# Kernel optimization log

Measured on AMD Instinct MI355X. Metric: run time of the kernel, lower is better.

The kernel has to match this reference:

```python
import jax, jax.numpy as jnp
import numpy as np

B, T, C, H, W = 4, 5, 64, 48, 48
F = 10                      # num_feat
N = T * H * W               # 11520, ffnn1 is Linear(N, N)


def setup_inputs() -> dict:
    key = jax.random.key(0)
    ks = jax.random.split(key, 9)
    sc = lambda *shape: 1.0 / np.sqrt(shape[-1])
    return {
        "input": jax.random.normal(ks[0], (B, T, C, H, W), jnp.float32),
        "input1": jax.random.normal(ks[1], (1,), jnp.float32),
        "act_weights": jax.random.uniform(ks[2], (3,), jnp.float32),
        # conv1: Conv1d(C, F, 1) -> weight [F, C] (kernel dim squeezed), bias [F]
        "conv1_w": jax.random.normal(ks[3], (F, C), jnp.float32) * sc(F, C),
        "conv1_b": jax.random.normal(ks[4], (F,), jnp.float32) * 0.01,
        # G3: Conv1d(C, F, 1)
        "g3_w": jax.random.normal(ks[5], (F, C), jnp.float32) * sc(F, C),
        "g3_b": jax.random.normal(ks[6], (F,), jnp.float32) * 0.01,
        # ffnn1: Linear(N, N)
        "ffnn_w": jax.random.normal(ks[7], (N, N), jnp.float32) * sc(N, N),
        "ffnn_b": jax.random.normal(ks[8], (N,), jnp.float32) * 0.01,
    }


def reference(input, input1, act_weights, conv1_w, conv1_b, g3_w, g3_b, ffnn_w, ffnn_b):
    b, t, c, h, w = input.shape
    n = t * h * w
    # [B, C, N]: transpose(1,2) then flatten T,H,W
    x = jnp.transpose(input, (0, 2, 1, 3, 4)).reshape(b, c, n)

    # conv1 (1x1) -> [B, F, N]; AvgPool1d(F) over the feat dim -> [B, N]
    c1 = jnp.einsum('bcn,fc->bfn', x, conv1_w) + conv1_b[None, :, None]
    s = jnp.mean(c1, axis=1)                      # [B, N]

    # ffnn1 (same Linear used in all three branches in the original)
    z = s @ ffnn_w.T + ffnn_b                     # [B, N]

    # G3 projection -> [B, N, F]
    g3 = jnp.einsum('bcn,fc->bnf', x, g3_w) + g3_b[None, None, :]

    # diag_embed(z) @ g3^T is exactly a per-position scale of g3 by z.
    gate = (act_weights[0] * jax.nn.relu(z)
            + act_weights[1] * jax.nn.sigmoid(z)
            + act_weights[2] * jax.nn.softmax(z, axis=1))  # [B, N]
    out = gate[:, :, None] * g3                   # [B, N, F]

    out = out.reshape(b, t, h, w, g3.shape[-1])   # [B, T, H, W, F]
    return jnp.transpose(out, (0, 1, 4, 2, 3))    # [B, T, F, H, W]
```

## Files before the change

kernel.cpp:

```cpp
#include <hip/hip_runtime.h>
#include <math.h>

#define Bsz 4
#define Tsz 5
#define Csz 64
#define Fsz 10
#define Hsz 48
#define Wsz 48
#define HWsz (Hsz*Wsz)
#define Nsz (Tsz*HWsz)

#define O_CWM 0
#define O_CBM 64
#define O_S   80
#define O_G3  (O_S + Bsz*Nsz)
#define O_Z   (O_G3 + Bsz*Fsz*Nsz)
#define O_MX  (O_Z + Bsz*Nsz)
#define O_SM  (O_MX + 4)

__global__ void k_prep(const float* __restrict__ cw, const float* __restrict__ cb,
                       float* __restrict__ ws) {
    int c = threadIdx.x;
    if (c < Csz) {
        float acc = 0.f;
        #pragma unroll
        for (int f = 0; f < Fsz; ++f) acc += cw[f*Csz + c];
        ws[O_CWM + c] = acc * (1.0f/Fsz);
    }
    if (c == 0) {
        float acc = 0.f;
        #pragma unroll
        for (int f = 0; f < Fsz; ++f) acc += cb[f];
        ws[O_CBM] = acc * (1.0f/Fsz);
    }
}

__global__ __launch_bounds__(64) void k_sg3(const float* __restrict__ in,
                                            const float* __restrict__ g3w,
                                            const float* __restrict__ g3b,
                                            float* __restrict__ ws) {
    __shared__ float sw[Fsz*Csz];
    __shared__ float scw[Csz + 1];
    for (int i = threadIdx.x; i < Fsz*Csz; i += 64) sw[i] = g3w[i];
    if (threadIdx.x < Csz) scw[threadIdx.x] = ws[O_CWM + threadIdx.x];
    if (threadIdx.x == 0) scw[Csz] = ws[O_CBM];
    __syncthreads();

    const int n = blockIdx.x * 64 + threadIdx.x;
    const int b = blockIdx.y;
    const int t = n / HWsz;
    const int p = n - t * HWsz;

    const float* xp = in + ((size_t)(b*Tsz + t) * Csz) * HWsz + p;

    float accs = 0.f;
    float accf[Fsz];
    #pragma unroll
    for (int f = 0; f < Fsz; ++f) accf[f] = 0.f;

    for (int c = 0; c < Csz; ++c) {
        float xv = xp[(size_t)c * HWsz];
        accs = fmaf(xv, scw[c], accs);
        #pragma unroll
        for (int f = 0; f < Fsz; ++f) accf[f] = fmaf(xv, sw[f*Csz + c], accf[f]);
    }

    float* s   = ws + O_S;
    float* g3t = ws + O_G3;
    s[b*Nsz + n] = accs + scw[Csz];
    #pragma unroll
    for (int f = 0; f < Fsz; ++f)
        g3t[((size_t)b*Fsz + f) * Nsz + n] = accf[f] + g3b[f];
}

__global__ __launch_bounds__(256) void k_gemv(const float* __restrict__ Wm,
                                              const float* __restrict__ fb,
                                              const float* __restrict__ ws) {
    const int wave = threadIdx.x >> 6;
    const int lane = threadIdx.x & 63;
    const int i = blockIdx.x * 4 + wave;

    const float4* wrow = (const float4*)(Wm + (size_t)i * Nsz);
    const float4* s4   = (const float4*)(ws + O_S);
    const int n4c = Nsz / 4;

    float a0 = 0.f, a1 = 0.f, a2 = 0.f, a3 = 0.f;
    for (int j = 0; j < Nsz/256; ++j) {
        const int n4 = j*64 + lane;
        float4 w4 = wrow[n4];
        float4 sv;
        sv = s4[0*n4c + n4];
        a0 = fmaf(w4.x, sv.x, a0); a0 = fmaf(w4.y, sv.y, a0);
        a0 = fmaf(w4.z, sv.z, a0); a0 = fmaf(w4.w, sv.w, a0);
        sv = s4[1*n4c + n4];
        a1 = fmaf(w4.x, sv.x, a1); a1 = fmaf(w4.y, sv.y, a1);
        a1 = fmaf(w4.z, sv.z, a1); a1 = fmaf(w4.w, sv.w, a1);
        sv = s4[2*n4c + n4];
        a2 = fmaf(w4.x, sv.x, a2); a2 = fmaf(w4.y, sv.y, a2);
        a2 = fmaf(w4.z, sv.z, a2); a2 = fmaf(w4.w, sv.w, a2);
        sv = s4[3*n4c + n4];
        a3 = fmaf(w4.x, sv.x, a3); a3 = fmaf(w4.y, sv.y, a3);
        a3 = fmaf(w4.z, sv.z, a3); a3 = fmaf(w4.w, sv.w, a3);
    }
    #pragma unroll
    for (int off = 32; off > 0; off >>= 1) {
        a0 += __shfl_xor(a0, off, 64);
        a1 += __shfl_xor(a1, off, 64);
        a2 += __shfl_xor(a2, off, 64);
        a3 += __shfl_xor(a3, off, 64);
    }
    if (lane == 0) {
        float bias = fb[i];
        float* z = (float*)ws + O_Z;
        z[0*Nsz + i] = a0 + bias;
        z[1*Nsz + i] = a1 + bias;
        z[2*Nsz + i] = a2 + bias;
        z[3*Nsz + i] = a3 + bias;
    }
}

__global__ __launch_bounds__(256) void k_stats(float* __restrict__ ws) {
    const int b = blockIdx.x;
    const float* zb = (const float*)ws + O_Z + (size_t)b * Nsz;
    const int lane = threadIdx.x & 63;
    const int wave = threadIdx.x >> 6;
    __shared__ float red[4];
    __shared__ float bcast;

    float m = -INFINITY;
    for (int i = threadIdx.x; i < Nsz; i += 256) m = fmaxf(m, zb[i]);
    #pragma unroll
    for (int off = 32; off > 0; off >>= 1) m = fmaxf(m, __shfl_xor(m, off, 64));
    if (lane == 0) red[wave] = m;
    __syncthreads();
    if (threadIdx.x == 0)
        bcast = fmaxf(fmaxf(red[0], red[1]), fmaxf(red[2], red[3]));
    __syncthreads();
    m = bcast;

    float sum = 0.f;
    for (int i = threadIdx.x; i < Nsz; i += 256) sum += expf(zb[i] - m);
    #pragma unroll
    for (int off = 32; off > 0; off >>= 1) sum += __shfl_xor(sum, off, 64);
    if (lane == 0) red[wave] = sum;
    __syncthreads();
    if (threadIdx.x == 0) {
        float* mx = ws + O_MX;
        float* sm = ws + O_SM;
        mx[b] = m;
        sm[b] = red[0] + red[1] + red[2] + red[3];
    }
}

__global__ __launch_bounds__(256) void k_out(const float* __restrict__ aw,
                                             const float* __restrict__ ws,
                                             float* __restrict__ out) {
    const int n = blockIdx.x * 256 + threadIdx.x;
    const int b = blockIdx.y;

    const float* z  = ws + O_Z;
    const float zv  = z[(size_t)b*Nsz + n];
    const float a0 = aw[0], a1 = aw[1], a2 = aw[2];
    const float mxb = ws[O_MX + b];
    const float smb = ws[O_SM + b];

    const float gate = a0 * fmaxf(zv, 0.f)
                     + a1 / (1.f + expf(-zv))
                     + a2 * expf(zv - mxb) / smb;

    const int t = n / HWsz;
    const int p = n - t * HWsz;
    const float* gp = ws + O_G3 + (size_t)b * Fsz * Nsz + n;
    float* ob = out + ((size_t)(b*Tsz + t) * Fsz) * HWsz + p;
    #pragma unroll
    for (int f = 0; f < Fsz; ++f)
        ob[(size_t)f * HWsz] = gate * gp[(size_t)f * Nsz];
}

extern "C" void kernel_launch(void* const* d_in, const int* in_sizes, int n_in,
                              void* d_out, int out_size, void* d_ws, size_t ws_size,
                              hipStream_t stream) {
    const float* input  = (const float*)d_in[0];
    const float* aw     = (const float*)d_in[2];
    const float* conv1w = (const float*)d_in[3];
    const float* conv1b = (const float*)d_in[4];
    const float* g3w    = (const float*)d_in[5];
    const float* g3b    = (const float*)d_in[6];
    const float* ffnw   = (const float*)d_in[7];
    const float* ffnb   = (const float*)d_in[8];
    float* out = (float*)d_out;
    float* ws  = (float*)d_ws;

    k_prep<<<1, 64, 0, stream>>>(conv1w, conv1b, ws);
    k_sg3<<<dim3(Nsz/64, Bsz), 64, 0, stream>>>(input, g3w, g3b, ws);
    k_gemv<<<Nsz/4, 256, 0, stream>>>(ffnw, ffnb, ws);
    k_stats<<<Bsz, 256, 0, stream>>>(ws);
    k_out<<<dim3(Nsz/256, Bsz), 256, 0, stream>>>(aw, ws, out);
}
```

Baseline: 769.7 us.

## Tile GEMV over rows with LDS-staged input vector and nontemporal weight loads

Each wave of the GEMV now computes four output rows, and each block stages chunks of the four batch vectors in shared memory. Those vectors are then reused across sixteen rows instead of being reread from global memory for every row. Weight rows are streamed with nontemporal loads. The prep kernel is folded into the projection kernel, which now uses 256-thread blocks, removing one launch. The cost is more registers and block-level syncs per chunk.

New measurement: 686.2 us. -10.9%, faster.

```diff
diff --git a/kernel.cpp b/kernel.cpp
--- a/kernel.cpp
+++ b/kernel.cpp
@@ -9,44 +9,42 @@
 #define Wsz 48
 #define HWsz (Hsz*Wsz)
 #define Nsz (Tsz*HWsz)
-
-#define O_CWM 0
-#define O_CBM 64
-#define O_S   80
+#define N4  (Nsz/4)
+#define KC4 576
+#define NCHUNK 5
+
+typedef float float4n __attribute__((ext_vector_type(4)));
+
+#define O_S   0
 #define O_G3  (O_S + Bsz*Nsz)
 #define O_Z   (O_G3 + Bsz*Fsz*Nsz)
 #define O_MX  (O_Z + Bsz*Nsz)
 #define O_SM  (O_MX + 4)
 
-__global__ void k_prep(const float* __restrict__ cw, const float* __restrict__ cb,
-                       float* __restrict__ ws) {
-    int c = threadIdx.x;
-    if (c < Csz) {
-        float acc = 0.f;
-        #pragma unroll
-        for (int f = 0; f < Fsz; ++f) acc += cw[f*Csz + c];
-        ws[O_CWM + c] = acc * (1.0f/Fsz);
-    }
-    if (c == 0) {
-        float acc = 0.f;
-        #pragma unroll
-        for (int f = 0; f < Fsz; ++f) acc += cb[f];
-        ws[O_CBM] = acc * (1.0f/Fsz);
-    }
-}
-
-__global__ __launch_bounds__(64) void k_sg3(const float* __restrict__ in,
-                                            const float* __restrict__ g3w,
-                                            const float* __restrict__ g3b,
-                                            float* __restrict__ ws) {
+__global__ __launch_bounds__(256) void k_sg3(const float* __restrict__ in,
+                                             const float* __restrict__ cw,
+                                             const float* __restrict__ cb,
+                                             const float* __restrict__ g3w,
+                                             const float* __restrict__ g3b,
+                                             float* __restrict__ ws) {
     __shared__ float sw[Fsz*Csz];
     __shared__ float scw[Csz + 1];
-    for (int i = threadIdx.x; i < Fsz*Csz; i += 64) sw[i] = g3w[i];
-    if (threadIdx.x < Csz) scw[threadIdx.x] = ws[O_CWM + threadIdx.x];
-    if (threadIdx.x == 0) scw[Csz] = ws[O_CBM];
-    __syncthreads();
-
-    const int n = blockIdx.x * 64 + threadIdx.x;
+    if (threadIdx.x < Csz) {
+        float a = 0.f;
+        #pragma unroll
+        for (int f = 0; f < Fsz; ++f) a += cw[f*Csz + threadIdx.x];
+        scw[threadIdx.x] = a * (1.0f/Fsz);
+    }
+    if (threadIdx.x == 0) {
+        float a = 0.f;
+        #pragma unroll
+        for (int f = 0; f < Fsz; ++f) a += cb[f];
+        scw[Csz] = a * (1.0f/Fsz);
+    }
+    for (int i = threadIdx.x; i < Fsz*Csz; i += 256) sw[i] = g3w[i];
+    __syncthreads();
+
+    const int n = blockIdx.x * 256 + threadIdx.x;
     const int b = blockIdx.y;
     const int t = n / HWsz;
     const int p = n - t * HWsz;
@@ -73,49 +71,84 @@
         g3t[((size_t)b*Fsz + f) * Nsz + n] = accf[f] + g3b[f];
 }
 
+#define DOT4(ACC, WV, SV) \
+    ACC = fmaf(WV.x, SV.x, ACC); ACC = fmaf(WV.y, SV.y, ACC); \
+    ACC = fmaf(WV.z, SV.z, ACC); ACC = fmaf(WV.w, SV.w, ACC)
+
 __global__ __launch_bounds__(256) void k_gemv(const float* __restrict__ Wm,
                                               const float* __restrict__ fb,
-                                              const float* __restrict__ ws) {
-    const int wave = threadIdx.x >> 6;
-    const int lane = threadIdx.x & 63;
-    const int i = blockIdx.x * 4 + wave;
-
-    const float4* wrow = (const float4*)(Wm + (size_t)i * Nsz);
-    const float4* s4   = (const float4*)(ws + O_S);
-    const int n4c = Nsz / 4;
-
-    float a0 = 0.f, a1 = 0.f, a2 = 0.f, a3 = 0.f;
-    for (int j = 0; j < Nsz/256; ++j) {
-        const int n4 = j*64 + lane;
-        float4 w4 = wrow[n4];
-        float4 sv;
-        sv = s4[0*n4c + n4];
-        a0 = fmaf(w4.x, sv.x, a0); a0 = fmaf(w4.y, sv.y, a0);
-        a0 = fmaf(w4.z, sv.z, a0); a0 = fmaf(w4.w, sv.w, a0);
-        sv = s4[1*n4c + n4];
-        a1 = fmaf(w4.x, sv.x, a1); a1 = fmaf(w4.y, sv.y, a1);
-        a1 = fmaf(w4.z, sv.z, a1); a1 = fmaf(w4.w, sv.w, a1);
-        sv = s4[2*n4c + n4];
-        a2 = fmaf(w4.x, sv.x, a2); a2 = fmaf(w4.y, sv.y, a2);
-        a2 = fmaf(w4.z, sv.z, a2); a2 = fmaf(w4.w, sv.w, a2);
-        sv = s4[3*n4c + n4];
-        a3 = fmaf(w4.x, sv.x, a3); a3 = fmaf(w4.y, sv.y, a3);
-        a3 = fmaf(w4.z, sv.z, a3); a3 = fmaf(w4.w, sv.w, a3);
-    }
-    #pragma unroll
-    for (int off = 32; off > 0; off >>= 1) {
-        a0 += __shfl_xor(a0, off, 64);
-        a1 += __shfl_xor(a1, off, 64);
-        a2 += __shfl_xor(a2, off, 64);
-        a3 += __shfl_xor(a3, off, 64);
-    }
+                                              float* __restrict__ ws) {
+    __shared__ float4 slds[Bsz][KC4];
+    const int tid  = threadIdx.x;
+    const int wave = tid >> 6;
+    const int lane = tid & 63;
+    const int row0 = blockIdx.x * 16 + wave * 4;
+
+    const float4n* w0 = (const float4n*)(Wm + (size_t)(row0    ) * Nsz);
+    const float4n* w1 = (const float4n*)(Wm + (size_t)(row0 + 1) * Nsz);
+    const float4n* w2 = (const float4n*)(Wm + (size_t)(row0 + 2) * Nsz);
+    const float4n* w3 = (const float4n*)(Wm + (size_t)(row0 + 3) * Nsz);
+    const float4* s4 = (const float4*)(ws + O_S);
+
+    float acc[4][4];
+    #pragma unroll
+    for (int r = 0; r < 4; ++r)
+        #pragma unroll
+        for (int b = 0; b < 4; ++b) acc[r][b] = 0.f;
+
+    for (int ch = 0; ch < NCHUNK; ++ch) {
+        const int c0 = ch * KC4;
+        __syncthreads();
+        #pragma unroll
+        for (int k = 0; k < (Bsz*KC4)/256; ++k) {
+            const int q = k*256 + tid;
+            const int b = q / KC4;
+            const int j = q - b * KC4;
+            slds[b][j] = s4[(size_t)b * N4 + c0 + j];
+        }
+        __syncthreads();
+
+        #pragma unroll
+        for (int jj = 0; jj < KC4/64; ++jj) {
+            const int j  = jj*64 + lane;
+            const int n4 = c0 + j;
+            const float4n a0 = __builtin_nontemporal_load(w0 + n4);
+            const float4n a1 = __builtin_nontemporal_load(w1 + n4);
+            const float4n a2 = __builtin_nontemporal_load(w2 + n4);
+            const float4n a3 = __builtin_nontemporal_load(w3 + n4);
+            float4 sv;
+            sv = slds[0][j];
+            DOT4(acc[0][0], a0, sv); DOT4(acc[1][0], a1, sv);
+            DOT4(acc[2][0], a2, sv); DOT4(acc[3][0], a3, sv);
+            sv = slds[1][j];
+            DOT4(acc[0][1], a0, sv); DOT4(acc[1][1], a1, sv);
+            DOT4(acc[2][1], a2, sv); DOT4(acc[3][1], a3, sv);
+            sv = slds[2][j];
+            DOT4(acc[0][2], a0, sv); DOT4(acc[1][2], a1, sv);
+            DOT4(acc[2][2], a2, sv); DOT4(acc[3][2], a3, sv);
+            sv = slds[3][j];
+            DOT4(acc[0][3], a0, sv); DOT4(acc[1][3], a1, sv);
+            DOT4(acc[2][3], a2, sv); DOT4(acc[3][3], a3, sv);
+        }
+    }
+
+    #pragma unroll
+    for (int r = 0; r < 4; ++r)
+        #pragma unroll
+        for (int b = 0; b < 4; ++b)
+            #pragma unroll
+            for (int off = 32; off > 0; off >>= 1)
+                acc[r][b] += __shfl_xor(acc[r][b], off, 64);
+
     if (lane == 0) {
-        float bias = fb[i];
-        float* z = (float*)ws + O_Z;
-        z[0*Nsz + i] = a0 + bias;
-        z[1*Nsz + i] = a1 + bias;
-        z[2*Nsz + i] = a2 + bias;
-        z[3*Nsz + i] = a3 + bias;
+        float* z = ws + O_Z;
+        #pragma unroll
+        for (int r = 0; r < 4; ++r) {
+            const float bias = fb[row0 + r];
+            #pragma unroll
+            for (int b = 0; b < 4; ++b)
+                z[(size_t)b*Nsz + row0 + r] = acc[r][b] + bias;
+        }
     }
 }
 
@@ -145,10 +178,8 @@
     if (lane == 0) red[wave] = sum;
     __syncthreads();
     if (threadIdx.x == 0) {
-        float* mx = ws + O_MX;
-        float* sm = ws + O_SM;
-        mx[b] = m;
-        sm[b] = red[0] + red[1] + red[2] + red[3];
+        ws[O_MX + b] = m;
+        ws[O_SM + b] = red[0] + red[1] + red[2] + red[3];
     }
 }
 
@@ -158,8 +189,7 @@
     const int n = blockIdx.x * 256 + threadIdx.x;
     const int b = blockIdx.y;
 
-    const float* z  = ws + O_Z;
-    const float zv  = z[(size_t)b*Nsz + n];
+    const float zv  = ws[O_Z + (size_t)b*Nsz + n];
     const float a0 = aw[0], a1 = aw[1], a2 = aw[2];
     const float mxb = ws[O_MX + b];
     const float smb = ws[O_SM + b];
@@ -191,9 +221,8 @@
     float* out = (float*)d_out;
     float* ws  = (float*)d_ws;
 
-    k_prep<<<1, 64, 0, stream>>>(conv1w, conv1b, ws);
-    k_sg3<<<dim3(Nsz/64, Bsz), 64, 0, stream>>>(input, g3w, g3b, ws);
-    k_gemv<<<Nsz/4, 256, 0, stream>>>(ffnw, ffnb, ws);
+    k_sg3  <<<dim3(Nsz/256, Bsz), 256, 0, stream>>>(input, conv1w, conv1b, g3w, g3b, ws);
+    k_gemv <<<Nsz/16, 256, 0, stream>>>(ffnw, ffnb, ws);
     k_stats<<<Bsz, 256, 0, stream>>>(ws);
-    k_out<<<dim3(Nsz/256, Bsz), 256, 0, stream>>>(aw, ws, out);
-}
+    k_out  <<<dim3(Nsz/256, Bsz), 256, 0, stream>>>(aw, ws, out);
+}
```
